# Kernel tuning notes

Hardware: AMD Instinct MI355X
Metric: run time of the kernel (lower is better)

The kernel has to match this reference:

```python
import jax, jax.numpy as jnp
import numpy as np

N = 100000   # nodes
E = 640000   # edges
D = 128      # feature dim
G = 512      # graphs in the batch


def setup_inputs() -> dict:
    key = jax.random.key(0)
    ks = jax.random.split(key, 6)
    x = jax.random.normal(ks[0], (N, D), dtype=jnp.float32)
    edge_index = jax.random.randint(ks[1], (2, E), 0, N, dtype=jnp.int32)
    batch = jnp.sort(jax.random.randint(ks[2], (N,), 0, G, dtype=jnp.int32))
    scale = 1.0 / np.sqrt(D)
    W0 = jax.random.normal(ks[3], (D, D), dtype=jnp.float32) * scale
    W1 = jax.random.normal(ks[4], (D, D), dtype=jnp.float32) * scale
    W2 = jax.random.normal(ks[5], (D, D), dtype=jnp.float32) * scale
    return {"x": x, "edge_index": edge_index, "batch": batch,
            "W0": W0, "W1": W1, "W2": W2}


def gcn_conv(x, W, row, col, n):
    """GCNConv (bias=False): x' = D^-1/2 (A + I) D^-1/2 (x @ W).
    row/col already include self-loops."""
    xw = x @ W                                              # [N, D]
    deg = jax.ops.segment_sum(jnp.ones_like(col, dtype=x.dtype), col,
                              num_segments=n)               # [N]
    dinv = jnp.where(deg > 0, jax.lax.rsqrt(deg), 0.0)
    norm = dinv[row] * dinv[col]                            # [E+N]
    msgs = norm[:, None] * xw[row]                          # gather + scale
    return jax.ops.segment_sum(msgs, col, num_segments=n)   # scatter-add


def reference(x, edge_index, batch, W0, W1, W2):
    n = x.shape[0]
    loops = jnp.arange(n, dtype=edge_index.dtype)
    row = jnp.concatenate([edge_index[0], loops])
    col = jnp.concatenate([edge_index[1], loops])
    # conv_layers[:-1] (no activation between them in forward)
    x = gcn_conv(x, W0, row, col, n)
    x = gcn_conv(x, W1, row, col, n)
    x = jax.nn.leaky_relu(x, negative_slope=0.01)
    x = gcn_conv(x, W2, row, col, n)
    # global_add_pool over graph ids
    return jax.ops.segment_sum(x, batch, num_segments=G)    # [G, D]
```

## Files before the change

### kernel.cpp

```cpp
#include <hip/hip_runtime.h>
#include <hip/hip_bf16.h>

#define FEAT 128

typedef unsigned int uint32;
typedef unsigned short ushort16;
typedef __attribute__((ext_vector_type(8))) short short8;
typedef __attribute__((ext_vector_type(4))) float v4f;
typedef __attribute__((ext_vector_type(2))) float f32x2;

__device__ __forceinline__ ushort16 f2bf(float f) {
    uint32 u = __float_as_uint(f);
    u += 0x7fffu + ((u >> 16) & 1u);
    return (ushort16)(u >> 16);
}
__device__ __forceinline__ float bflo(uint32 u) { return __uint_as_float(u << 16); }
__device__ __forceinline__ float bfhi(uint32 u) { return __uint_as_float(u & 0xffff0000u); }
__device__ __forceinline__ f32x2 up2(uint32 u) { return (f32x2){bflo(u), bfhi(u)}; }

__device__ __forceinline__ void gemm_body(const float* __restrict__ A,
                                          const ushort16* __restrict__ Wt,
                                          ushort16* __restrict__ Ch, int n,
                                          int pairId, int pairStride,
                                          int tile0, int tile1, int t) {
    const int w = t >> 6;
    const int lane = t & 63;
    const int quad = lane >> 4;
    const int l16 = lane & 15;
    const int colBase = (w & 1) * 64;

    short8 wf[4][4];
#pragma unroll
    for (int ct = 0; ct < 4; ct++) {
        const ushort16* wp = Wt + (size_t)(colBase + ct * 16 + l16) * FEAT + quad * 8;
#pragma unroll
        for (int ks = 0; ks < 4; ks++) wf[ct][ks] = *(const short8*)(wp + ks * 32);
    }

    int tile = tile0 + pairId;
    if (tile >= tile1) return;

    auto loadA = [&](int tl, short8 (&a)[4]) {
        const int rowi = tl * 16 + l16;
        if (rowi < n) {
#pragma unroll
            for (int ks = 0; ks < 4; ks++) {
                const float* ap = A + (size_t)rowi * FEAT + quad * 8 + ks * 32;
                float4 f0 = *(const float4*)ap;
                float4 f1 = *(const float4*)(ap + 4);
                short8 v;
                v[0] = f2bf(f0.x); v[1] = f2bf(f0.y); v[2] = f2bf(f0.z); v[3] = f2bf(f0.w);
                v[4] = f2bf(f1.x); v[5] = f2bf(f1.y); v[6] = f2bf(f1.z); v[7] = f2bf(f1.w);
                a[ks] = v;
            }
        } else {
#pragma unroll
            for (int ks = 0; ks < 4; ks++) a[ks] = (short8)0;
        }
    };

    short8 aCur[4];
    loadA(tile, aCur);

    while (tile < tile1) {
        const int nextTile = tile + pairStride;
        short8 aNxt[4];
        if (nextTile < tile1) loadA(nextTile, aNxt);

        v4f acc[4];
#pragma unroll
        for (int ct = 0; ct < 4; ct++) acc[ct] = (v4f)0.f;
#pragma unroll
        for (int ct = 0; ct < 4; ct++)
#pragma unroll
            for (int ks = 0; ks < 4; ks++)
                acc[ct] = __builtin_amdgcn_mfma_f32_16x16x32_bf16(wf[ct][ks], aCur[ks], acc[ct], 0, 0, 0);

        const int rowi = tile * 16 + l16;
        if (rowi < n) {
#pragma unroll
            for (int ct = 0; ct < 4; ct++) {
                uint2 o;
                o.x = (uint32)f2bf(acc[ct][0]) | ((uint32)f2bf(acc[ct][1]) << 16);
                o.y = (uint32)f2bf(acc[ct][2]) | ((uint32)f2bf(acc[ct][3]) << 16);
                *(uint2*)(Ch + (size_t)rowi * FEAT + colBase + ct * 16 + quad * 4) = o;
            }
        }

        tile = nextTile;
#pragma unroll
        for (int ks = 0; ks < 4; ks++) aCur[ks] = aNxt[ks];
    }
}

__global__ __launch_bounds__(256) void pre_kernel(int* __restrict__ counts, int n,
                                                  const float* __restrict__ W0,
                                                  const float* __restrict__ W1,
                                                  ushort16* __restrict__ W01t,
                                                  float* __restrict__ Pbuf) {
    int b = blockIdx.x;
    int t = threadIdx.x;
    if (b < 100) {
        int idx = (b * 256 + t) * 4;
        if (idx + 3 < n) {
            *(int4*)(counts + idx) = make_int4(0, 0, 0, 0);
        } else {
            for (int i = idx; i < n; i++) counts[i] = 0;
        }
    } else if (b < 164) {
        __shared__ float sW0[2][FEAT];
        int wb = b - 100;
        int lk = t >> 7;
        int ncol = t & 127;
        int k = wb * 2 + lk;
        sW0[lk][ncol] = W0[(size_t)k * FEAT + ncol];
        __syncthreads();
        float acc = 0.f;
#pragma unroll 4
        for (int j = 0; j < FEAT; j++)
            acc += sW0[lk][j] * W1[(size_t)j * FEAT + ncol];
        W01t[(size_t)ncol * FEAT + k] = f2bf(acc);
    } else {
        int zb = b - 164;
        float4 z = make_float4(0.f, 0.f, 0.f, 0.f);
        float* p = Pbuf + (size_t)zb * 2048 + t * 8;
        *(float4*)p = z;
        *(float4*)(p + 4) = z;
    }
}

__global__ __launch_bounds__(256) void histgemmA_kernel(const int* __restrict__ col,
                                                        int* __restrict__ counts, int E,
                                                        const float* __restrict__ A,
                                                        const ushort16* __restrict__ Wt,
                                                        ushort16* __restrict__ Ch, int n) {
    const int b = blockIdx.x;
    const int r9 = b % 9;
    const int g9 = b / 9;
    const int t = threadIdx.x;
    if (r9 >= 4) {
        int hb = g9 * 5 + (r9 - 4);
        int id = hb * 256 + t;
        if (id * 4 + 3 < E) {
            int4 c4 = *(const int4*)(col + id * 4);
            atomicAdd(&counts[c4.x], 1);
            atomicAdd(&counts[c4.y], 1);
            atomicAdd(&counts[c4.z], 1);
            atomicAdd(&counts[c4.w], 1);
        } else {
            for (int e = id * 4; e < E; e++) atomicAdd(&counts[col[e]], 1);
        }
        return;
    }
    int gb = g9 * 4 + r9;
    gemm_body(A, Wt, Ch, n, gb * 2 + ((t >> 6) >> 1), 1024, 0, 3125, t);
}

__global__ __launch_bounds__(256) void scan_part(const int* __restrict__ counts,
                                                 int* __restrict__ bsum, int n) {
    __shared__ int s[256];
    int base = blockIdx.x * 1024;
    int t = threadIdx.x;
    int v = 0;
#pragma unroll
    for (int i = 0; i < 4; i++) {
        int idx = base + t * 4 + i;
        if (idx < n) v += counts[idx];
    }
    s[t] = v;
    __syncthreads();
    for (int o = 128; o > 0; o >>= 1) {
        if (t < o) s[t] += s[t + o];
        __syncthreads();
    }
    if (t == 0) bsum[blockIdx.x] = s[0];
}

__global__ __launch_bounds__(256) void scan_final(const int* __restrict__ counts,
                                                  const int* __restrict__ bsum,
                                                  int* __restrict__ off, int* __restrict__ nxt,
                                                  float* __restrict__ dinv, int n, int nb) {
    __shared__ int s[256];
    __shared__ int sb[128];
    int base = blockIdx.x * 1024;
    int t = threadIdx.x;
    if (t < nb) sb[t] = bsum[t];
    int c[4];
    int sum = 0;
#pragma unroll
    for (int i = 0; i < 4; i++) {
        int idx = base + t * 4 + i;
        c[i] = (idx < n) ? counts[idx] : 0;
        sum += c[i];
    }
    int v0 = sum;
    s[t] = sum;
    __syncthreads();
    for (int o = 1; o < 256; o <<= 1) {
        int v = (t >= o) ? s[t - o] : 0;
        __syncthreads();
        s[t] += v;
        __syncthreads();
    }
    int blockBase = 0;
    for (int j = 0; j < blockIdx.x; j++) blockBase += sb[j];
    int excl = s[t] - v0 + blockBase;
#pragma unroll
    for (int i = 0; i < 4; i++) {
        int idx = base + t * 4 + i;
        if (idx < n) {
            off[idx] = excl;
            nxt[idx] = excl;
            dinv[idx] = rsqrtf((float)(c[i] + 1));
        }
        excl += c[i];
    }
    if (blockIdx.x == gridDim.x - 1 && t == 255) off[n] = excl;
}

__global__ __launch_bounds__(256) void fillgemmB_kernel(const float* __restrict__ A,
                                                        const ushort16* __restrict__ Wt,
                                                        ushort16* __restrict__ Ch, int n,
                                                        const int* __restrict__ row,
                                                        const int* __restrict__ col,
                                                        int* __restrict__ nxt,
                                                        int* __restrict__ srcArr, int E) {
    const int b = blockIdx.x;
    const int r7 = b % 7;
    const int g7 = b / 7;
    const int t = threadIdx.x;
    if (r7 >= 2) {
        int fb = g7 * 5 + (r7 - 2);
        int e = fb * 256 + t;
        if (e < E) {
            int c = col[e], r = row[e];
            int p = atomicAdd(&nxt[c], 1);
            __builtin_nontemporal_store(r, &srcArr[p]);
        }
        return;
    }
    int gb = g7 * 2 + r7;
    gemm_body(A, Wt, Ch, n, gb * 2 + ((t >> 6) >> 1), 2048, 3125, 6250, t);
}

__global__ __launch_bounds__(256) void gather_kernel(const int* __restrict__ off,
                                                     const int* __restrict__ srcArr,
                                                     const float* __restrict__ dinv,
                                                     const ushort16* __restrict__ XWh,
                                                     ushort16* __restrict__ Hh, int n,
                                                     int leaky) {
    int node = blockIdx.x * 4 + (threadIdx.x >> 6);
    if (node >= n) return;
    int lane = threadIdx.x & 63;
    int grp = lane >> 4;
    int l16 = lane & 15;
    float dc = dinv[node];
    const uint4* table = (const uint4*)XWh;

    f32x2 acc[4];
    if (grp == 0) {
        uint4 v = table[(size_t)node * 16 + l16];
        f32x2 w0 = (f32x2){dc * dc, dc * dc};
        acc[0] = w0 * up2(v.x);
        acc[1] = w0 * up2(v.y);
        acc[2] = w0 * up2(v.z);
        acc[3] = w0 * up2(v.w);
    } else {
#pragma unroll
        for (int j = 0; j < 4; j++) acc[j] = (f32x2){0.f, 0.f};
    }

    int s = off[node], e = off[node + 1];
    int i = s + grp;
    for (; i + 4 < e; i += 8) {
        int r0 = srcArr[i];
        int r1 = srcArr[i + 4];
        uint4 u0 = table[(size_t)r0 * 16 + l16];
        uint4 u1 = table[(size_t)r1 * 16 + l16];
        float f0 = dc * dinv[r0];
        float f1 = dc * dinv[r1];
        f32x2 n0 = (f32x2){f0, f0};
        f32x2 n1 = (f32x2){f1, f1};
        acc[0] += n0 * up2(u0.x);
        acc[1] += n0 * up2(u0.y);
        acc[2] += n0 * up2(u0.z);
        acc[3] += n0 * up2(u0.w);
        acc[0] += n1 * up2(u1.x);
        acc[1] += n1 * up2(u1.y);
        acc[2] += n1 * up2(u1.z);
        acc[3] += n1 * up2(u1.w);
    }
    if (i < e) {
        int r0 = srcArr[i];
        uint4 u0 = table[(size_t)r0 * 16 + l16];
        float f0 = dc * dinv[r0];
        f32x2 n0 = (f32x2){f0, f0};
        acc[0] += n0 * up2(u0.x);
        acc[1] += n0 * up2(u0.y);
        acc[2] += n0 * up2(u0.z);
        acc[3] += n0 * up2(u0.w);
    }

    float b[8] = {acc[0].x, acc[0].y, acc[1].x, acc[1].y,
                  acc[2].x, acc[2].y, acc[3].x, acc[3].y};
#pragma unroll
    for (int j = 0; j < 8; j++) {
        b[j] += __shfl_xor(b[j], 16);
        b[j] += __shfl_xor(b[j], 32);
    }

    if (grp == 0) {
        if (leaky) {
#pragma unroll
            for (int j = 0; j < 8; j++) b[j] = (b[j] >= 0.f) ? b[j] : 0.01f * b[j];
        }
        uint4 o;
        o.x = (uint32)f2bf(b[0]) | ((uint32)f2bf(b[1]) << 16);
        o.y = (uint32)f2bf(b[2]) | ((uint32)f2bf(b[3]) << 16);
        o.z = (uint32)f2bf(b[4]) | ((uint32)f2bf(b[5]) << 16);
        o.w = (uint32)f2bf(b[6]) | ((uint32)f2bf(b[7]) << 16);
        *(uint4*)(Hh + (size_t)node * FEAT + l16 * 8) = o;
    }
}

__global__ __launch_bounds__(128) void pool_kernel(const ushort16* __restrict__ H,
                                                   const int* __restrict__ batch,
                                                   float* __restrict__ P, int n) {
    int t = threadIdx.x;
    int i0 = blockIdx.x * 32;
    if (i0 >= n) return;
    int i1 = min(i0 + 32, n);
    float acc = 0.f;
    int g = batch[i0];
    for (int i = i0; i < i1; i++) {
        int b = batch[i];
        if (b != g) {
            atomicAdd(&P[(size_t)g * FEAT + t], acc);
            acc = 0.f;
            g = b;
        }
        uint32 u = (uint32)(unsigned short)H[(size_t)i * FEAT + t];
        acc += __uint_as_float(u << 16);
    }
    atomicAdd(&P[(size_t)g * FEAT + t], acc);
}

__global__ __launch_bounds__(128) void pgemm_kernel(const float* __restrict__ P,
                                                    const float* __restrict__ W2,
                                                    float* __restrict__ out) {
    __shared__ float sP[FEAT];
    const int g = blockIdx.x;
    const int t = threadIdx.x;
    sP[t] = P[(size_t)g * FEAT + t];
    __syncthreads();
    float o = 0.f;
#pragma unroll 4
    for (int k = 0; k < FEAT; k++) o += sP[k] * W2[(size_t)k * FEAT + t];
    out[(size_t)g * FEAT + t] = o;
}

extern "C" void kernel_launch(void* const* d_in, const int* in_sizes, int n_in,
                              void* d_out, int out_size, void* d_ws, size_t ws_size,
                              hipStream_t stream) {
    const float* x = (const float*)d_in[0];
    const int* ei = (const int*)d_in[1];
    const int* batch = (const int*)d_in[2];
    const float* W0 = (const float*)d_in[3];
    const float* W1 = (const float*)d_in[4];
    const float* W2 = (const float*)d_in[5];
    float* out = (float*)d_out;

    const int N = in_sizes[0] / FEAT;
    const int E = in_sizes[1] / 2;
    const int G = out_size / FEAT;

    const int* rowI = ei;
    const int* colI = ei + E;

    char* ws = (char*)d_ws;
    auto take = [&](size_t bytes) {
        char* p = ws;
        ws += (bytes + 15) & ~(size_t)15;
        return p;
    };
    int* counts    = (int*)take((size_t)N * 4);
    int* off       = (int*)take((size_t)(N + 1) * 4);
    int* nxt       = (int*)take((size_t)N * 4);
    float* dinv    = (float*)take((size_t)N * 4);
    int* bsum      = (int*)take(128 * 4);
    int* srcArr    = (int*)take((size_t)E * 4);
    ushort16* W01t = (ushort16*)take((size_t)16384 * 2);
    float* Pbuf    = (float*)take((size_t)G * FEAT * 4);
    ushort16* bufA = (ushort16*)take((size_t)N * FEAT * 2);
    ushort16* bufB = (ushort16*)take((size_t)N * FEAT * 2);

    const int nb = (N + 1023) / 1024;

    pre_kernel<<<196, 256, 0, stream>>>(counts, N, W0, W1, W01t, Pbuf);

    histgemmA_kernel<<<128 * 9, 256, 0, stream>>>(colI, counts, E, x, W01t, bufA, N);

    scan_part<<<nb, 256, 0, stream>>>(counts, bsum, N);
    scan_final<<<nb, 256, 0, stream>>>(counts, bsum, off, nxt, dinv, N, nb);

    fillgemmB_kernel<<<512 * 7, 256, 0, stream>>>(x, W01t, bufA, N,
                                                  rowI, colI, nxt, srcArr, E);

    const int gatBlocks = (N + 3) / 4;
    gather_kernel<<<gatBlocks, 256, 0, stream>>>(off, srcArr, dinv, bufA, bufB, N, 0);
    gather_kernel<<<gatBlocks, 256, 0, stream>>>(off, srcArr, dinv, bufB, bufA, N, 1);
    gather_kernel<<<gatBlocks, 256, 0, stream>>>(off, srcArr, dinv, bufA, bufB, N, 0);
    pool_kernel<<<(N + 31) / 32, 128, 0, stream>>>(bufB, batch, Pbuf, N);
    pgemm_kernel<<<G, 128, 0, stream>>>(Pbuf, W2, out);
}
```

Before: 332.2 us.

## Fold source-side normalization into stored features and fuse pooling into last gather

Each gather now stores features already scaled by dinv of the destination node, squared so they also carry the next layer's source factor. Later layers can then sum neighbor rows without loading dinv[r] per edge. The third gather skips writing its node features and instead reduces its four nodes per block in shared memory and atomically adds them into the per-graph pool buffer, which removes the separate pool kernel and one full feature-matrix write and read. The cost is a block-wide sync plus more atomics in the last layer, and a change in where bf16 rounding happens relative to the normalization.

```diff
diff --git a/kernel.cpp b/kernel.cpp
--- a/kernel.cpp
+++ b/kernel.cpp
@@ -243,106 +243,150 @@
     gemm_body(A, Wt, Ch, n, gb * 2 + ((t >> 6) >> 1), 2048, 3125, 6250, t);
 }
 
+template <int MODE>
 __global__ __launch_bounds__(256) void gather_kernel(const int* __restrict__ off,
                                                      const int* __restrict__ srcArr,
                                                      const float* __restrict__ dinv,
-                                                     const ushort16* __restrict__ XWh,
-                                                     ushort16* __restrict__ Hh, int n,
-                                                     int leaky) {
-    int node = blockIdx.x * 4 + (threadIdx.x >> 6);
-    if (node >= n) return;
-    int lane = threadIdx.x & 63;
-    int grp = lane >> 4;
-    int l16 = lane & 15;
-    float dc = dinv[node];
-    const uint4* table = (const uint4*)XWh;
-
-    f32x2 acc[4];
-    if (grp == 0) {
-        uint4 v = table[(size_t)node * 16 + l16];
-        f32x2 w0 = (f32x2){dc * dc, dc * dc};
-        acc[0] = w0 * up2(v.x);
-        acc[1] = w0 * up2(v.y);
-        acc[2] = w0 * up2(v.z);
-        acc[3] = w0 * up2(v.w);
+                                                     const uint4* __restrict__ table,
+                                                     ushort16* __restrict__ Hh,
+                                                     const int* __restrict__ batch,
+                                                     float* __restrict__ P, int n) {
+    const int t = threadIdx.x;
+    const int wid = t >> 6;
+    const int node = blockIdx.x * 4 + wid;
+    const int lane = t & 63;
+    const int grp = lane >> 4;
+    const int l16 = lane & 15;
+    const bool valid = node < n;
+
+    float b[8];
+    float dc = 0.f;
+    if (valid) {
+        dc = dinv[node];
+        f32x2 acc[4];
+        if (grp == 0) {
+            uint4 v = table[(size_t)node * 16 + l16];
+            if (MODE == 0) {
+                f32x2 w0 = (f32x2){dc, dc};
+                acc[0] = w0 * up2(v.x);
+                acc[1] = w0 * up2(v.y);
+                acc[2] = w0 * up2(v.z);
+                acc[3] = w0 * up2(v.w);
+            } else {
+                acc[0] = up2(v.x);
+                acc[1] = up2(v.y);
+                acc[2] = up2(v.z);
+                acc[3] = up2(v.w);
+            }
+        } else {
+#pragma unroll
+            for (int j = 0; j < 4; j++) acc[j] = (f32x2){0.f, 0.f};
+        }
+
+        int s = off[node], e = off[node + 1];
+        int i = s + grp;
+        if (MODE == 0) {
+            for (; i + 4 < e; i += 8) {
+                int r0 = srcArr[i];
+                int r1 = srcArr[i + 4];
+                uint4 u0 = table[(size_t)r0 * 16 + l16];
+                uint4 u1 = table[(size_t)r1 * 16 + l16];
+                float f0 = dinv[r0];
+                float f1 = dinv[r1];
+                f32x2 n0 = (f32x2){f0, f0};
+                f32x2 n1 = (f32x2){f1, f1};
+                acc[0] += n0 * up2(u0.x);
+                acc[1] += n0 * up2(u0.y);
+                acc[2] += n0 * up2(u0.z);
+                acc[3] += n0 * up2(u0.w);
+                acc[0] += n1 * up2(u1.x);
+                acc[1] += n1 * up2(u1.y);
+                acc[2] += n1 * up2(u1.z);
+                acc[3] += n1 * up2(u1.w);
+            }
+            if (i < e) {
+                int r0 = srcArr[i];
+                uint4 u0 = table[(size_t)r0 * 16 + l16];
+                float f0 = dinv[r0];
+                f32x2 n0 = (f32x2){f0, f0};
+                acc[0] += n0 * up2(u0.x);
+                acc[1] += n0 * up2(u0.y);
+                acc[2] += n0 * up2(u0.z);
+                acc[3] += n0 * up2(u0.w);
+            }
+        } else {
+            for (; i + 4 < e; i += 8) {
+                int r0 = srcArr[i];
+                int r1 = srcArr[i + 4];
+                uint4 u0 = table[(size_t)r0 * 16 + l16];
+                uint4 u1 = table[(size_t)r1 * 16 + l16];
+                acc[0] += up2(u0.x) + up2(u1.x);
+                acc[1] += up2(u0.y) + up2(u1.y);
+                acc[2] += up2(u0.z) + up2(u1.z);
+                acc[3] += up2(u0.w) + up2(u1.w);
+            }
+            if (i < e) {
+                int r0 = srcArr[i];
+                uint4 u0 = table[(size_t)r0 * 16 + l16];
+                acc[0] += up2(u0.x);
+                acc[1] += up2(u0.y);
+                acc[2] += up2(u0.z);
+                acc[3] += up2(u0.w);
+            }
+        }
+
+        b[0] = acc[0].x; b[1] = acc[0].y; b[2] = acc[1].x; b[3] = acc[1].y;
+        b[4] = acc[2].x; b[5] = acc[2].y; b[6] = acc[3].x; b[7] = acc[3].y;
+#pragma unroll
+        for (int j = 0; j < 8; j++) {
+            b[j] += __shfl_xor(b[j], 16);
+            b[j] += __shfl_xor(b[j], 32);
+        }
+    }
+
+    if constexpr (MODE == 2) {
+        __shared__ float sB[4][FEAT];
+        __shared__ int sG[4];
+        if (lane == 0) sG[wid] = valid ? batch[node] : -1;
+        if (valid && grp == 0) {
+#pragma unroll
+            for (int j = 0; j < 8; j++) sB[wid][l16 * 8 + j] = dc * b[j];
+        }
+        __syncthreads();
+        if (t < FEAT) {
+            int g0 = sG[0], g1 = sG[1], g2 = sG[2], g3 = sG[3];
+            if (g0 == g1 && g1 == g2 && g2 == g3 && g0 >= 0) {
+                atomicAdd(&P[(size_t)g0 * FEAT + t],
+                          sB[0][t] + sB[1][t] + sB[2][t] + sB[3][t]);
+            } else {
+                if (g0 >= 0) atomicAdd(&P[(size_t)g0 * FEAT + t], sB[0][t]);
+                if (g1 >= 0) atomicAdd(&P[(size_t)g1 * FEAT + t], sB[1][t]);
+                if (g2 >= 0) atomicAdd(&P[(size_t)g2 * FEAT + t], sB[2][t]);
+                if (g3 >= 0) atomicAdd(&P[(size_t)g3 * FEAT + t], sB[3][t]);
+            }
+        }
     } else {
-#pragma unroll
-        for (int j = 0; j < 4; j++) acc[j] = (f32x2){0.f, 0.f};
-    }
-
-    int s = off[node], e = off[node + 1];
-    int i = s + grp;
-    for (; i + 4 < e; i += 8) {
-        int r0 = srcArr[i];
-        int r1 = srcArr[i + 4];
-        uint4 u0 = table[(size_t)r0 * 16 + l16];
-        uint4 u1 = table[(size_t)r1 * 16 + l16];
-        float f0 = dc * dinv[r0];
-        float f1 = dc * dinv[r1];
-        f32x2 n0 = (f32x2){f0, f0};
-        f32x2 n1 = (f32x2){f1, f1};
-        acc[0] += n0 * up2(u0.x);
-        acc[1] += n0 * up2(u0.y);
-        acc[2] += n0 * up2(u0.z);
-        acc[3] += n0 * up2(u0.w);
-        acc[0] += n1 * up2(u1.x);
-        acc[1] += n1 * up2(u1.y);
-        acc[2] += n1 * up2(u1.z);
-        acc[3] += n1 * up2(u1.w);
-    }
-    if (i < e) {
-        int r0 = srcArr[i];
-        uint4 u0 = table[(size_t)r0 * 16 + l16];
-        float f0 = dc * dinv[r0];
-        f32x2 n0 = (f32x2){f0, f0};
-        acc[0] += n0 * up2(u0.x);
-        acc[1] += n0 * up2(u0.y);
-        acc[2] += n0 * up2(u0.z);
-        acc[3] += n0 * up2(u0.w);
-    }
-
-    float b[8] = {acc[0].x, acc[0].y, acc[1].x, acc[1].y,
-                  acc[2].x, acc[2].y, acc[3].x, acc[3].y};
-#pragma unroll
-    for (int j = 0; j < 8; j++) {
-        b[j] += __shfl_xor(b[j], 16);
-        b[j] += __shfl_xor(b[j], 32);
-    }
-
-    if (grp == 0) {
-        if (leaky) {
-#pragma unroll
-            for (int j = 0; j < 8; j++) b[j] = (b[j] >= 0.f) ? b[j] : 0.01f * b[j];
-        }
-        uint4 o;
-        o.x = (uint32)f2bf(b[0]) | ((uint32)f2bf(b[1]) << 16);
-        o.y = (uint32)f2bf(b[2]) | ((uint32)f2bf(b[3]) << 16);
-        o.z = (uint32)f2bf(b[4]) | ((uint32)f2bf(b[5]) << 16);
-        o.w = (uint32)f2bf(b[6]) | ((uint32)f2bf(b[7]) << 16);
-        *(uint4*)(Hh + (size_t)node * FEAT + l16 * 8) = o;
-    }
-}
-
-__global__ __launch_bounds__(128) void pool_kernel(const ushort16* __restrict__ H,
-                                                   const int* __restrict__ batch,
-                                                   float* __restrict__ P, int n) {
-    int t = threadIdx.x;
-    int i0 = blockIdx.x * 32;
-    if (i0 >= n) return;
-    int i1 = min(i0 + 32, n);
-    float acc = 0.f;
-    int g = batch[i0];
-    for (int i = i0; i < i1; i++) {
-        int b = batch[i];
-        if (b != g) {
-            atomicAdd(&P[(size_t)g * FEAT + t], acc);
-            acc = 0.f;
-            g = b;
-        }
-        uint32 u = (uint32)(unsigned short)H[(size_t)i * FEAT + t];
-        acc += __uint_as_float(u << 16);
-    }
-    atomicAdd(&P[(size_t)g * FEAT + t], acc);
+        if (valid && grp == 0) {
+            float sc = dc * dc;
+            if (MODE == 1) {
+#pragma unroll
+                for (int j = 0; j < 8; j++) {
+                    float h = b[j];
+                    h = (h >= 0.f) ? h : 0.01f * h;
+                    b[j] = sc * h;
+                }
+            } else {
+#pragma unroll
+                for (int j = 0; j < 8; j++) b[j] *= sc;
+            }
+            uint4 o;
+            o.x = (uint32)f2bf(b[0]) | ((uint32)f2bf(b[1]) << 16);
+            o.y = (uint32)f2bf(b[2]) | ((uint32)f2bf(b[3]) << 16);
+            o.z = (uint32)f2bf(b[4]) | ((uint32)f2bf(b[5]) << 16);
+            o.w = (uint32)f2bf(b[6]) | ((uint32)f2bf(b[7]) << 16);
+            *(uint4*)(Hh + (size_t)node * FEAT + l16 * 8) = o;
+        }
+    }
 }
 
 __global__ __launch_bounds__(128) void pgemm_kernel(const float* __restrict__ P,
@@ -407,9 +451,14 @@
                                                   rowI, colI, nxt, srcArr, E);
 
     const int gatBlocks = (N + 3) / 4;
-    gather_kernel<<<gatBlocks, 256, 0, stream>>>(off, srcArr, dinv, bufA, bufB, N, 0);
-    gather_kernel<<<gatBlocks, 256, 0, stream>>>(off, srcArr, dinv, bufB, bufA, N, 1);
-    gather_kernel<<<gatBlocks, 256, 0, stream>>>(off, srcArr, dinv, bufA, bufB, N, 0);
-    pool_kernel<<<(N + 31) / 32, 128, 0, stream>>>(bufB, batch, Pbuf, N);
+    gather_kernel<0><<<gatBlocks, 256, 0, stream>>>(off, srcArr, dinv,
+                                                    (const uint4*)bufA, bufB,
+                                                    nullptr, nullptr, N);
+    gather_kernel<1><<<gatBlocks, 256, 0, stream>>>(off, srcArr, dinv,
+                                                    (const uint4*)bufB, bufA,
+                                                    nullptr, nullptr, N);
+    gather_kernel<2><<<gatBlocks, 256, 0, stream>>>(off, srcArr, dinv,
+                                                    (const uint4*)bufA, nullptr,
+                                                    batch, Pbuf, N);
     pgemm_kernel<<<G, 128, 0, stream>>>(Pbuf, W2, out);
 }
```

Measured after the change: 326.4 us. Within noise of the previous version (-1.7%).
